# Kernel optimization log

Measured on AMD Instinct MI355X. Metric: run time of the kernel, lower is better.

Reference implementation:

```python
import jax, jax.numpy as jnp
import numpy as np

N_ROWS = 65536  # number of rows of the sparse input matrix


def setup_inputs() -> dict:
    key = jax.random.key(0)
    k1, k2, k3, k4, k5 = jax.random.split(key, 5)
    nnz, d_in, d_out = 524288, 512, 512
    rows = jax.random.randint(k1, (nnz,), 0, N_ROWS, dtype=jnp.int64)
    cols = jax.random.randint(k2, (nnz,), 0, d_in, dtype=jnp.int64)
    values = jax.random.normal(k3, (nnz,), dtype=jnp.float32)
    weight = jax.random.normal(k4, (d_out, d_in), dtype=jnp.float32) * (1.0 / np.sqrt(d_in))
    bound = 1.0 / np.sqrt(d_in)
    bias = jax.random.uniform(k5, (d_out,), minval=-bound, maxval=bound, dtype=jnp.float32)
    return {"rows": rows, "cols": cols, "values": values, "weight": weight, "bias": bias}


def reference(rows, cols, values, weight, bias):
    # y = sparse_input @ weight.T + bias
    # Each nonzero (r, c, v) contributes v * weight[:, c] to output row r.
    # weight: [d_out, d_in]; gather columns -> [nnz, d_out], segment-sum by row.
    contrib = values[:, None] * weight.T[cols]          # [nnz, d_out]
    y = jax.ops.segment_sum(contrib, rows, num_segments=N_ROWS)  # [N, d_out]
    return y + bias
```

## Files before the change

kernel.cpp:

```cpp
#include <hip/hip_runtime.h>
#include <hip/hip_bf16.h>

#define D 512
#define NROWS 65536
#define NBINS 512
#define RPB 128
#define P1B 1024
#define SEGCAP 12
#define MAXBLK1 512
#define BINCAP 1408
#define OVFCAP 4096

typedef float f32x4 __attribute__((ext_vector_type(4)));

__global__ __launch_bounds__(256) void k_phase1(const float* __restrict__ w,
                                                __hip_bfloat16* __restrict__ wt,
                                                const int* __restrict__ rows,
                                                const int* __restrict__ cols,
                                                const float* __restrict__ vals, int nnz, int nblk1,
                                                uint2* __restrict__ gBin, int* __restrict__ gBinCnt,
                                                int* __restrict__ ovf_cnt, uint4* __restrict__ ovf) {
    int b = blockIdx.x, t = threadIdx.x;
    if (b < 256) {
        __shared__ float tile[32][33];
        if (b == 0 && t == 0) *ovf_cnt = 0;
        int bx = b & 15, by = b >> 4;
        int tx = t & 31, ty = t >> 5;
        for (int i = ty; i < 32; i += 8)
            tile[i][tx] = w[(by * 32 + i) * D + bx * 32 + tx];
        __syncthreads();
        for (int i = ty; i < 32; i += 8)
            wt[(bx * 32 + i) * D + by * 32 + tx] = __float2bfloat16(tile[tx][i]);
        return;
    }
    __shared__ int  binCnt[NBINS];
    __shared__ uint2 binBuf[NBINS][SEGCAP];
    b -= 256;
    binCnt[t] = 0;
    binCnt[t + 256] = 0;
    __syncthreads();
    int base = b * P1B;
    int end = base + P1B; if (end > nnz) end = nnz;
    for (int i = base + t; i < end; i += 256) {
        int r = rows[i], c = cols[i];
        unsigned vb = __float_as_uint(vals[i]);
        int bin = r >> 7;
        int pos = atomicAdd(&binCnt[bin], 1);
        if (pos < SEGCAP) {
            binBuf[bin][pos] = make_uint2(((unsigned)r << 9) | (unsigned)c, vb);
        } else {
            int o = atomicAdd(ovf_cnt, 1);
            if (o < OVFCAP) ovf[o] = make_uint4((unsigned)r, (unsigned)c, vb, 0u);
        }
    }
    __syncthreads();
    for (int idx = t; idx < NBINS * SEGCAP; idx += 256) {
        int bin = idx / SEGCAP, slot = idx - bin * SEGCAP;
        int cnt = binCnt[bin]; if (cnt > SEGCAP) cnt = SEGCAP;
        if (slot < cnt)
            gBin[((size_t)b * NBINS + bin) * SEGCAP + slot] = binBuf[bin][slot];
        if (slot == 0) gBinCnt[b * NBINS + bin] = cnt;
    }
}

#define ACC8(wb, vv)                                   \
    do {                                               \
        f32x4 w0, w1;                                  \
        w0.x = __uint_as_float((wb).x << 16);          \
        w0.y = __uint_as_float((wb).x & 0xffff0000u);  \
        w0.z = __uint_as_float((wb).y << 16);          \
        w0.w = __uint_as_float((wb).y & 0xffff0000u);  \
        w1.x = __uint_as_float((wb).z << 16);          \
        w1.y = __uint_as_float((wb).z & 0xffff0000u);  \
        w1.z = __uint_as_float((wb).w << 16);          \
        w1.w = __uint_as_float((wb).w & 0xffff0000u);  \
        a0 += (vv) * w0;                               \
        a1 += (vv) * w1;                               \
    } while (0)

__global__ __launch_bounds__(512) void k_binspmm(const uint2* __restrict__ gBin,
                                                 const int* __restrict__ gBinCnt, int nblk1,
                                                 const uint4* __restrict__ wt4,
                                                 const f32x4* __restrict__ bias4,
                                                 f32x4* __restrict__ out,
                                                 int* __restrict__ ovf_cnt,
                                                 uint4* __restrict__ ovf) {
    __shared__ int segCnt[MAXBLK1], segOff[MAXBLK1];
    __shared__ int rowCnt[RPB], rowOff[RPB], cursor[RPB];
    __shared__ int wsum[8], wsum2[2];
    __shared__ uint2 pairBuf[BINCAP];
    __shared__ uint2 csrBuf[BINCAP];
    int bin = blockIdx.x, t = threadIdx.x;
    int wv = t >> 6, lane = t & 63;
    int sc = (t < nblk1) ? gBinCnt[t * NBINS + bin] : 0;
    int x = sc;
    for (int d = 1; d < 64; d <<= 1) {
        int y = __shfl_up(x, d, 64);
        if (lane >= d) x += y;
    }
    if (lane == 63) wsum[wv] = x;
    if (t < RPB) rowCnt[t] = 0;
    __syncthreads();
    int woff = 0, total = 0;
#pragma unroll
    for (int k = 0; k < 8; ++k) {
        int s = wsum[k];
        if (k < wv) woff += s;
        total += s;
    }
    segOff[t] = x - sc + woff;
    segCnt[t] = sc;
    if (total > BINCAP) total = BINCAP;
    __syncthreads();
    for (int idx = t; idx < nblk1 * SEGCAP; idx += 512) {
        int blk = idx / SEGCAP, slot = idx - blk * SEGCAP;
        if (slot < segCnt[blk]) {
            int dst = segOff[blk] + slot;
            uint2 p = gBin[((size_t)blk * NBINS + bin) * SEGCAP + slot];
            if (dst < BINCAP) {
                pairBuf[dst] = p;
                atomicAdd(&rowCnt[(p.x >> 9) & (RPB - 1)], 1);
            } else {
                int o = atomicAdd(ovf_cnt, 1);
                if (o < OVFCAP)
                    ovf[o] = make_uint4(p.x >> 9, p.x & 511u, p.y, 0u);
            }
        }
    }
    __syncthreads();
    int rc = (t < RPB) ? rowCnt[t] : 0;
    int rx = rc;
    for (int d = 1; d < 64; d <<= 1) {
        int y = __shfl_up(rx, d, 64);
        if (lane >= d) rx += y;
    }
    if (t < RPB && lane == 63) wsum2[wv] = rx;
    __syncthreads();
    if (t < RPB) {
        int ro = rx - rc + ((wv == 1) ? wsum2[0] : 0);
        rowOff[t] = ro;
        cursor[t] = ro;
    }
    __syncthreads();
    for (int k = t; k < total; k += 512) {
        uint2 p = pairBuf[k];
        int r = (p.x >> 9) & (RPB - 1);
        int pos = atomicAdd(&cursor[r], 1);
        csrBuf[pos] = make_uint2(p.x & 511u, p.y);
    }
    __syncthreads();
    f32x4 bb0 = bias4[lane * 2];
    f32x4 bb1 = bias4[lane * 2 + 1];
    int novf = *ovf_cnt;
    if (novf > OVFCAP) novf = OVFCAP;
    for (int rloc = wv; rloc < RPB; rloc += 8) {
        int cnt = rowCnt[rloc], o = rowOff[rloc];
        f32x4 a0 = bb0, a1 = bb1;
        for (int s = 0; s < cnt; s += 4) {
            int i1 = (s + 1 < cnt) ? s + 1 : s;
            int i2 = (s + 2 < cnt) ? s + 2 : s;
            int i3 = (s + 3 < cnt) ? s + 3 : s;
            uint2 p0 = csrBuf[o + s];
            uint2 p1 = csrBuf[o + i1];
            uint2 p2 = csrBuf[o + i2];
            uint2 p3 = csrBuf[o + i3];
            float v0 = __uint_as_float(p0.y);
            float v1 = (s + 1 < cnt) ? __uint_as_float(p1.y) : 0.f;
            float v2 = (s + 2 < cnt) ? __uint_as_float(p2.y) : 0.f;
            float v3 = (s + 3 < cnt) ? __uint_as_float(p3.y) : 0.f;
            uint4 wb0 = wt4[(size_t)p0.x * 64 + lane];
            uint4 wb1 = wt4[(size_t)p1.x * 64 + lane];
            uint4 wb2 = wt4[(size_t)p2.x * 64 + lane];
            uint4 wb3 = wt4[(size_t)p3.x * 64 + lane];
            ACC8(wb0, v0);
            ACC8(wb1, v1);
            ACC8(wb2, v2);
            ACC8(wb3, v3);
        }
        int row = (bin << 7) + rloc;
        if (novf > 0) {
            for (int e = 0; e < novf; ++e) {
                uint4 p = ovf[e];
                if ((int)p.x == row) {
                    float v = __uint_as_float(p.z);
                    uint4 wb = wt4[(size_t)p.y * 64 + lane];
                    ACC8(wb, v);
                }
            }
        }
        f32x4* op = out + (size_t)row * (D / 4);
        op[lane * 2]     = a0;
        op[lane * 2 + 1] = a1;
    }
}

__global__ void k_init_bias(const float* __restrict__ bias, float* __restrict__ out, int total) {
    int i = blockIdx.x * blockDim.x + threadIdx.x;
    if (i < total) out[i] = bias[i & (D - 1)];
}

__global__ void k_atomic_spmm(const int* __restrict__ rows, const int* __restrict__ cols,
                              const float* __restrict__ vals, int nnz,
                              const float* __restrict__ w, float* __restrict__ out) {
    int wid = (int)((blockIdx.x * blockDim.x + threadIdx.x) >> 6);
    if (wid >= nnz) return;
    int lane = threadIdx.x & 63;
    int r = rows[wid];
    int c = cols[wid];
    float v = vals[wid];
    float* op = out + (size_t)r * D + lane * 8;
#pragma unroll
    for (int k = 0; k < 8; ++k) {
        float wv = w[(size_t)(lane * 8 + k) * D + c];
        atomicAdd(&op[k], v * wv);
    }
}

extern "C" void kernel_launch(void* const* d_in, const int* in_sizes, int n_in,
                              void* d_out, int out_size, void* d_ws, size_t ws_size,
                              hipStream_t stream) {
    const int*   rows   = (const int*)d_in[0];
    const int*   cols   = (const int*)d_in[1];
    const float* vals   = (const float*)d_in[2];
    const float* weight = (const float*)d_in[3];
    const float* bias   = (const float*)d_in[4];
    float*       out    = (float*)d_out;
    const int nnz = in_sizes[0];
    const int nblk1 = (nnz + P1B - 1) / P1B;

    char* ws = (char*)d_ws;
    size_t off = 0;
    auto alloc = [&](size_t bytes) -> void* {
        off = (off + 255) & ~(size_t)255;
        void* p = ws + off;
        off += bytes;
        return p;
    };
    __hip_bfloat16* wT = (__hip_bfloat16*)alloc((size_t)D * D * sizeof(__hip_bfloat16));
    int*   ovf_cnt = (int*)  alloc(256);
    uint4* ovf     = (uint4*)alloc((size_t)OVFCAP * sizeof(uint4));
    uint2* gBin    = (uint2*)alloc((size_t)MAXBLK1 * NBINS * SEGCAP * sizeof(uint2));
    int*   gBinCnt = (int*)  alloc((size_t)MAXBLK1 * NBINS * sizeof(int));
    const size_t need_full = off;

    if (need_full <= ws_size && nblk1 <= MAXBLK1) {
        k_phase1<<<256 + nblk1, 256, 0, stream>>>(weight, wT, rows, cols, vals, nnz, nblk1,
                                                  gBin, gBinCnt, ovf_cnt, ovf);
        k_binspmm<<<NBINS, 512, 0, stream>>>(gBin, gBinCnt, nblk1, (const uint4*)wT,
                                             (const f32x4*)bias, (f32x4*)out, ovf_cnt, ovf);
    } else {
        k_init_bias<<<(out_size + 255) / 256, 256, 0, stream>>>(bias, out, out_size);
        k_atomic_spmm<<<((size_t)nnz * 64 + 255) / 256, 256, 0, stream>>>(rows, cols, vals, nnz, weight, out);
    }
}
```

Measured before the change: 60.87 us.

## Coarsen phase-1 bins to 256 rows and split each bin across two blocks

Phase 1 now bins nonzeros into 256 coarse bins of 256 rows, each with 16 slots per segment. This halves the per-block bin count and turns the index divide into a shift. The SpMM kernel launches two blocks per coarse bin, and each block filters out the pairs for its own 128-row half. That replaces the per-segment prefix scan with a shared atomic counter. The trade-off is that each SpMM block reads twice as many gBin entries and throws away half of them, and the overflow counter reset moves into a separate memset call.

```diff
diff --git a/kernel.cpp b/kernel.cpp
--- a/kernel.cpp
+++ b/kernel.cpp
@@ -3,12 +3,12 @@
 
 #define D 512
 #define NROWS 65536
-#define NBINS 512
+#define NBINS 256
 #define RPB 128
 #define P1B 1024
-#define SEGCAP 12
+#define SEGCAP 16
 #define MAXBLK1 512
-#define BINCAP 1408
+#define HBINCAP 1408
 #define OVFCAP 4096
 
 typedef float f32x4 __attribute__((ext_vector_type(4)));
@@ -23,7 +23,6 @@
     int b = blockIdx.x, t = threadIdx.x;
     if (b < 256) {
         __shared__ float tile[32][33];
-        if (b == 0 && t == 0) *ovf_cnt = 0;
         int bx = b & 15, by = b >> 4;
         int tx = t & 31, ty = t >> 5;
         for (int i = ty; i < 32; i += 8)
@@ -37,14 +36,13 @@
     __shared__ uint2 binBuf[NBINS][SEGCAP];
     b -= 256;
     binCnt[t] = 0;
-    binCnt[t + 256] = 0;
     __syncthreads();
     int base = b * P1B;
     int end = base + P1B; if (end > nnz) end = nnz;
     for (int i = base + t; i < end; i += 256) {
         int r = rows[i], c = cols[i];
         unsigned vb = __float_as_uint(vals[i]);
-        int bin = r >> 7;
+        int bin = r >> 8;
         int pos = atomicAdd(&binCnt[bin], 1);
         if (pos < SEGCAP) {
             binBuf[bin][pos] = make_uint2(((unsigned)r << 9) | (unsigned)c, vb);
@@ -55,7 +53,7 @@
     }
     __syncthreads();
     for (int idx = t; idx < NBINS * SEGCAP; idx += 256) {
-        int bin = idx / SEGCAP, slot = idx - bin * SEGCAP;
+        int bin = idx >> 4, slot = idx & (SEGCAP - 1);
         int cnt = binCnt[bin]; if (cnt > SEGCAP) cnt = SEGCAP;
         if (slot < cnt)
             gBin[((size_t)b * NBINS + bin) * SEGCAP + slot] = binBuf[bin][slot];
@@ -85,49 +83,39 @@
                                                  f32x4* __restrict__ out,
                                                  int* __restrict__ ovf_cnt,
                                                  uint4* __restrict__ ovf) {
-    __shared__ int segCnt[MAXBLK1], segOff[MAXBLK1];
+    __shared__ int segCnt[MAXBLK1];
     __shared__ int rowCnt[RPB], rowOff[RPB], cursor[RPB];
-    __shared__ int wsum[8], wsum2[2];
-    __shared__ uint2 pairBuf[BINCAP];
-    __shared__ uint2 csrBuf[BINCAP];
-    int bin = blockIdx.x, t = threadIdx.x;
+    __shared__ int wsum2[2];
+    __shared__ int nPairs;
+    __shared__ uint2 pairBuf[HBINCAP];
+    __shared__ uint2 csrBuf[HBINCAP];
+    int bin = blockIdx.x >> 1, half = blockIdx.x & 1;
+    int t = threadIdx.x;
     int wv = t >> 6, lane = t & 63;
-    int sc = (t < nblk1) ? gBinCnt[t * NBINS + bin] : 0;
-    int x = sc;
-    for (int d = 1; d < 64; d <<= 1) {
-        int y = __shfl_up(x, d, 64);
-        if (lane >= d) x += y;
-    }
-    if (lane == 63) wsum[wv] = x;
+    segCnt[t] = (t < nblk1) ? gBinCnt[t * NBINS + bin] : 0;
     if (t < RPB) rowCnt[t] = 0;
-    __syncthreads();
-    int woff = 0, total = 0;
-#pragma unroll
-    for (int k = 0; k < 8; ++k) {
-        int s = wsum[k];
-        if (k < wv) woff += s;
-        total += s;
-    }
-    segOff[t] = x - sc + woff;
-    segCnt[t] = sc;
-    if (total > BINCAP) total = BINCAP;
+    if (t == 0) nPairs = 0;
     __syncthreads();
     for (int idx = t; idx < nblk1 * SEGCAP; idx += 512) {
-        int blk = idx / SEGCAP, slot = idx - blk * SEGCAP;
+        int blk = idx >> 4, slot = idx & (SEGCAP - 1);
         if (slot < segCnt[blk]) {
-            int dst = segOff[blk] + slot;
             uint2 p = gBin[((size_t)blk * NBINS + bin) * SEGCAP + slot];
-            if (dst < BINCAP) {
-                pairBuf[dst] = p;
-                atomicAdd(&rowCnt[(p.x >> 9) & (RPB - 1)], 1);
-            } else {
-                int o = atomicAdd(ovf_cnt, 1);
-                if (o < OVFCAP)
-                    ovf[o] = make_uint4(p.x >> 9, p.x & 511u, p.y, 0u);
+            int localr = (int)((p.x >> 9) & 255u);
+            if ((localr >> 7) == half) {
+                int dst = atomicAdd(&nPairs, 1);
+                if (dst < HBINCAP) {
+                    pairBuf[dst] = p;
+                    atomicAdd(&rowCnt[localr & (RPB - 1)], 1);
+                } else {
+                    int o = atomicAdd(ovf_cnt, 1);
+                    if (o < OVFCAP)
+                        ovf[o] = make_uint4(p.x >> 9, p.x & 511u, p.y, 0u);
+                }
             }
         }
     }
     __syncthreads();
+    int total = nPairs; if (total > HBINCAP) total = HBINCAP;
     int rc = (t < RPB) ? rowCnt[t] : 0;
     int rx = rc;
     for (int d = 1; d < 64; d <<= 1) {
@@ -144,7 +132,7 @@
     __syncthreads();
     for (int k = t; k < total; k += 512) {
         uint2 p = pairBuf[k];
-        int r = (p.x >> 9) & (RPB - 1);
+        int r = (int)(p.x >> 9) & (RPB - 1);
         int pos = atomicAdd(&cursor[r], 1);
         csrBuf[pos] = make_uint2(p.x & 511u, p.y);
     }
@@ -177,7 +165,7 @@
             ACC8(wb2, v2);
             ACC8(wb3, v3);
         }
-        int row = (bin << 7) + rloc;
+        int row = (bin << 8) + (half << 7) + rloc;
         if (novf > 0) {
             for (int e = 0; e < novf; ++e) {
                 uint4 p = ovf[e];
@@ -244,10 +232,11 @@
     const size_t need_full = off;
 
     if (need_full <= ws_size && nblk1 <= MAXBLK1) {
+        hipMemsetAsync(ovf_cnt, 0, sizeof(int), stream);
         k_phase1<<<256 + nblk1, 256, 0, stream>>>(weight, wT, rows, cols, vals, nnz, nblk1,
                                                   gBin, gBinCnt, ovf_cnt, ovf);
-        k_binspmm<<<NBINS, 512, 0, stream>>>(gBin, gBinCnt, nblk1, (const uint4*)wT,
-                                             (const f32x4*)bias, (f32x4*)out, ovf_cnt, ovf);
+        k_binspmm<<<NBINS * 2, 512, 0, stream>>>(gBin, gBinCnt, nblk1, (const uint4*)wT,
+                                                 (const f32x4*)bias, (f32x4*)out, ovf_cnt, ovf);
     } else {
         k_init_bias<<<(out_size + 255) / 256, 256, 0, stream>>>(bias, out, out_size);
         k_atomic_spmm<<<((size_t)nnz * 64 + 255) / 256, 256, 0, stream>>>(rows, cols, vals, nnz, weight, out);
```

After: 64.27 us. 1.06x slower.
